# Kernel tuning notes

Measured on AMD Instinct MI355X. Metric: run time of the kernel, lower is better.

## Reference

```python
import jax, jax.numpy as jnp
import numpy as np

COLB = 16            # COL_BLOCK_WIDTH
IN_W = 1024          # input_width; zero_inputs=0 so input_locations = arange(IN_W)
OUT_W = 512          # output_width
DEPTH = 8            # network_depth
IN_L = 4             # butterfly_in_depth
OUT_L = 4            # butterfly_out_depth
ACT = 8              # activations_per_block
BLOCKS = 64          # blocks_per_layer -> num_inputs = 1024 per module
CURV = 1.0
GROW = BLOCKS * ACT  # 512 new rows per module
TOTAL = IN_W + DEPTH * GROW  # 5120
BATCH = 4096


def setup_inputs() -> dict:
    key = jax.random.key(0)
    k1, k2, k3 = jax.random.split(key, 3)
    input_data = jax.random.normal(k1, (IN_W, BATCH), dtype=jnp.float32)
    scales = jnp.full((IN_W,), 0.05, dtype=jnp.float32)
    # angles uniform in (-pi, pi), shape [depth, in_layers+out_layers, num_inputs/2]
    angles = (jax.random.uniform(k2, (DEPTH, IN_L + OUT_L, BLOCKS * COLB // 2)) * 2.0 - 1.0) * np.pi
    angles = angles.astype(jnp.float32)
    biases = jax.random.normal(k3, (DEPTH, GROW), dtype=jnp.float32) * 0.05
    # per-module indices_in = randperm(total_width_so_far)[:num_inputs]
    rng = np.random.RandomState(0)
    tw = IN_W
    idxs = []
    for _ in range(DEPTH):
        idxs.append(rng.permutation(tw)[: BLOCKS * COLB].astype(np.int32))
        tw += GROW
    indices_in = jnp.asarray(np.stack(idxs))  # [depth, 1024]
    return {"input_data": input_data, "scales": scales, "angles": angles,
            "biases": biases, "indices_in": indices_in}


def _rotate(x, ang, stride):
    # x: [W, B]; pair row i (with (i//stride)%2==0) with row i+stride inside 16-blocks
    W, B = x.shape
    xr = x.reshape(W // (2 * stride), 2, stride, B)
    a = ang.reshape(W // (2 * stride), stride)[:, :, None]
    c, s = jnp.cos(a), jnp.sin(a)
    lo, hi = xr[:, 0], xr[:, 1]              # [W/2s, s, B]
    nlo = c * lo + s * hi
    nhi = -s * lo + c * hi
    return jnp.stack([nlo, nhi], axis=1).reshape(W, B)


def _butterfly_module(data, ang, bias, idx, idx_out):
    W = BLOCKS * COLB
    x = data[idx]                             # gather [1024, B]
    for l in range(IN_L):
        x = _rotate(x, ang[l], 2 ** (l % 4))
    xb = x.reshape(BLOCKS, COLB, -1)
    pre = xb[:, :ACT, :] + bias.reshape(BLOCKS, ACT)[:, :, None]
    # curvature (smoothed-ReLU) activation
    act = 0.5 * (pre + jnp.sqrt(pre * pre + CURV * CURV))
    xb = xb.at[:, :ACT, :].set(act)
    x = xb.reshape(W, -1)
    for l in range(OUT_L):
        x = _rotate(x, ang[IN_L + l], 2 ** ((IN_L + l) % 4))
    data = data.at[idx].set(x)                # scatter working set back
    data = data.at[idx_out: idx_out + GROW].set(act.reshape(GROW, -1))
    return data


def reference(input_data, scales, angles, biases, indices_in):
    B = input_data.shape[1]
    data = jnp.zeros((TOTAL, B), dtype=input_data.dtype)
    data = data.at[:IN_W].set(scales[:, None] * input_data)
    for i in range(DEPTH):
        data = _butterfly_module(data, angles[i], biases[i], indices_in[i], IN_W + GROW * i)
    return data[TOTAL - OUT_W:]
```

## Files before the change

kernel.cpp:

```cpp
#include <hip/hip_runtime.h>
#include <math.h>

#define N_INW     1024
#define N_DEPTH   8
#define N_GROW    512
#define N_BATCH   4096
#define N_THREADS 128
#define N_LAYERS  64

typedef __attribute__((ext_vector_type(2))) float F2;
typedef decltype(__builtin_amdgcn_cvt_pkrtz(0.f, 0.f)) H2;

__global__ void precompute_cs_kernel(const float* __restrict__ angles,
                                     float* __restrict__ cs) {
    int i = blockIdx.x * blockDim.x + threadIdx.x;
    if (i < N_LAYERS * 512) {
        int g = i >> 9, p = i & 511;
        float a = angles[i];
        cs[(2 * g) * 512 + p]     = cosf(a);
        cs[(2 * g + 1) * 512 + p] = sinf(a);
    }
}

#define ADDR(r) (((r) << 3) + ((((r) >> 4)) << 2) + cpo)

#define LD2(A) ({ H2 _h = *(const H2*)(L + (A));                               \
                  F2 _v; _v.x = (float)_h.x; _v.y = (float)_h.y; _v; })
#define ST2(A, V) do { F2 _w = (V);                                            \
    *(H2*)(L + (A)) = __builtin_amdgcn_cvt_pkrtz(_w.x, _w.y); } while (0)

#define LDCS(g, CA, CB, SA, SB) do { if (USE_TABLE) {                          \
    const float4* _c = (const float4*)(cs_tab + (2*(g))*512 + (blk<<3));       \
    const float4* _s = (const float4*)(cs_tab + (2*(g)+1)*512 + (blk<<3));     \
    CA = _c[0]; CB = _c[1]; SA = _s[0]; SB = _s[1];                            \
  } else {                                                                     \
    const float4* _p = (const float4*)(angles + (g)*512 + (blk<<3));           \
    float4 _a = _p[0], _b = _p[1];                                             \
    __sincosf(_a.x, &SA.x, &CA.x); __sincosf(_a.y, &SA.y, &CA.y);              \
    __sincosf(_a.z, &SA.z, &CA.z); __sincosf(_a.w, &SA.w, &CA.w);              \
    __sincosf(_b.x, &SB.x, &CB.x); __sincosf(_b.y, &SB.y, &CB.y);              \
    __sincosf(_b.z, &SB.z, &CB.z); __sincosf(_b.w, &SB.w, &CB.w);              \
  } } while (0)

#define ROTP(LO, HI, CC, SS) do { F2 _l = LO, _h = HI;                         \
    LO = CC * _l + SS * _h; HI = CC * _h - SS * _l; } while (0)

#define ROTS1(CA,CB,SA,SB) do {                                                \
    ROTP(x0,x1,CA.x,SA.x);  ROTP(x2,x3,CA.y,SA.y);                             \
    ROTP(x4,x5,CA.z,SA.z);  ROTP(x6,x7,CA.w,SA.w);                             \
    ROTP(x8,x9,CB.x,SB.x);  ROTP(x10,x11,CB.y,SB.y);                           \
    ROTP(x12,x13,CB.z,SB.z);ROTP(x14,x15,CB.w,SB.w); } while (0)
#define ROTS2(CA,CB,SA,SB) do {                                                \
    ROTP(x0,x2,CA.x,SA.x);  ROTP(x1,x3,CA.y,SA.y);                             \
    ROTP(x4,x6,CA.z,SA.z);  ROTP(x5,x7,CA.w,SA.w);                             \
    ROTP(x8,x10,CB.x,SB.x); ROTP(x9,x11,CB.y,SB.y);                            \
    ROTP(x12,x14,CB.z,SB.z);ROTP(x13,x15,CB.w,SB.w); } while (0)
#define ROTS4(CA,CB,SA,SB) do {                                                \
    ROTP(x0,x4,CA.x,SA.x);  ROTP(x1,x5,CA.y,SA.y);                             \
    ROTP(x2,x6,CA.z,SA.z);  ROTP(x3,x7,CA.w,SA.w);                             \
    ROTP(x8,x12,CB.x,SB.x); ROTP(x9,x13,CB.y,SB.y);                            \
    ROTP(x10,x14,CB.z,SB.z);ROTP(x11,x15,CB.w,SB.w); } while (0)
#define ROTS8(CA,CB,SA,SB) do {                                                \
    ROTP(x0,x8,CA.x,SA.x);  ROTP(x1,x9,CA.y,SA.y);                             \
    ROTP(x2,x10,CA.z,SA.z); ROTP(x3,x11,CA.w,SA.w);                            \
    ROTP(x4,x12,CB.x,SB.x); ROTP(x5,x13,CB.y,SB.y);                            \
    ROTP(x6,x14,CB.z,SB.z); ROTP(x7,x15,CB.w,SB.w); } while (0)

#define ACT1(X, BB) do { F2 _p = (X) + (BB);                                   \
    F2 _t = _p * _p + 1.0f;                                                    \
    F2 _r; _r.x = __builtin_amdgcn_sqrtf(_t.x);                                \
    _r.y = __builtin_amdgcn_sqrtf(_t.y);                                       \
    X = 0.5f * (_p + _r); } while (0)

#define MODULE(M) {                                                            \
  const int a0=ADDR(i0.x), a1=ADDR(i0.y), a2=ADDR(i0.z), a3=ADDR(i0.w),        \
            a4=ADDR(i1.x), a5=ADDR(i1.y), a6=ADDR(i1.z), a7=ADDR(i1.w),        \
            a8=ADDR(i2.x), a9=ADDR(i2.y), a10=ADDR(i2.z), a11=ADDR(i2.w),      \
            a12=ADDR(i3.x), a13=ADDR(i3.y), a14=ADDR(i3.z), a15=ADDR(i3.w);    \
  float4 cA,cB,sA,sB, dA,dB,tA,tB, eA,eB,uA,uB, ba,bb;                         \
  LDCS(8*(M)+0, cA,cB,sA,sB);                                                  \
  LDCS(8*(M)+1, dA,dB,tA,tB);                                                  \
  F2 x0=LD2(a0), x1=LD2(a1), x2=LD2(a2), x3=LD2(a3);                           \
  F2 x4=LD2(a4), x5=LD2(a5), x6=LD2(a6), x7=LD2(a7);                           \
  F2 x8=LD2(a8), x9=LD2(a9), x10=LD2(a10), x11=LD2(a11);                       \
  F2 x12=LD2(a12), x13=LD2(a13), x14=LD2(a14), x15=LD2(a15);                   \
  LDCS(8*(M)+2, eA,eB,uA,uB);                                                  \
  { const float4* _bp = (const float4*)(biases + (M)*N_GROW + (blk<<3));       \
    ba = _bp[0]; bb = _bp[1]; }                                                \
  ROTS1(cA,cB,sA,sB);                                                          \
  LDCS(8*(M)+3, cA,cB,sA,sB);                                                  \
  ROTS2(dA,dB,tA,tB);                                                          \
  ROTS4(eA,eB,uA,uB);                                                          \
  ROTS8(cA,cB,sA,sB);                                                          \
  ACT1(x0,ba.x); ACT1(x1,ba.y); ACT1(x2,ba.z); ACT1(x3,ba.w);                  \
  ACT1(x4,bb.x); ACT1(x5,bb.y); ACT1(x6,bb.z); ACT1(x7,bb.w);                  \
  if ((M) < 7) {                                                               \
                            \
    const int _br = N_INW + (M)*N_GROW + (blk<<3);                             \
    const int _ab = ADDR(_br);                                                 \
    ST2(_ab+ 0,x0); ST2(_ab+ 8,x1); ST2(_ab+16,x2); ST2(_ab+24,x3);            \
    ST2(_ab+32,x4); ST2(_ab+40,x5); ST2(_ab+48,x6); ST2(_ab+56,x7);            \
                                           \
    { const int4* _ip = (const int4*)(indices + ((M)+1)*N_INW + (blk<<4));     \
      i0=_ip[0]; i1=_ip[1]; i2=_ip[2]; i3=_ip[3]; }                            \
    LDCS(8*(M)+4, dA,dB,tA,tB);                                                \
    LDCS(8*(M)+5, eA,eB,uA,uB);                                                \
    ROTS1(dA,dB,tA,tB);                                                        \
    LDCS(8*(M)+6, dA,dB,tA,tB);                                                \
    ROTS2(eA,eB,uA,uB);                                                        \
    LDCS(8*(M)+7, eA,eB,uA,uB);                                                \
    ROTS4(dA,dB,tA,tB);                                                        \
    ROTS8(eA,eB,uA,uB);                                                        \
    ST2(a0,x0);  ST2(a1,x1);  ST2(a2,x2);  ST2(a3,x3);                         \
    ST2(a4,x4);  ST2(a5,x5);  ST2(a6,x6);  ST2(a7,x7);                         \
    ST2(a8,x8);  ST2(a9,x9);  ST2(a10,x10); ST2(a11,x11);                      \
    ST2(a12,x12); ST2(a13,x13); ST2(a14,x14); ST2(a15,x15);                    \
  } else {                                                                     \
        \
    *(F2*)(out + (size_t)((blk<<3)+0)*N_BATCH + cg) = x0;                      \
    *(F2*)(out + (size_t)((blk<<3)+1)*N_BATCH + cg) = x1;                      \
    *(F2*)(out + (size_t)((blk<<3)+2)*N_BATCH + cg) = x2;                      \
    *(F2*)(out + (size_t)((blk<<3)+3)*N_BATCH + cg) = x3;                      \
    *(F2*)(out + (size_t)((blk<<3)+4)*N_BATCH + cg) = x4;                      \
    *(F2*)(out + (size_t)((blk<<3)+5)*N_BATCH + cg) = x5;                      \
    *(F2*)(out + (size_t)((blk<<3)+6)*N_BATCH + cg) = x6;                      \
    *(F2*)(out + (size_t)((blk<<3)+7)*N_BATCH + cg) = x7;                      \
  } }

template <bool USE_TABLE>
__global__ __launch_bounds__(N_THREADS, 1)
void butterfly_fused_kernel(const float* __restrict__ input,
                            const float* __restrict__ scales,
                            const float* __restrict__ biases,
                            const int*   __restrict__ indices,
                            const float* __restrict__ cs_tab,
                            const float* __restrict__ angles,
                            float* __restrict__ out) {
    extern __shared__ float ldsbuf[];
    char* L = (char*)ldsbuf;
    const int t   = threadIdx.x;
    const int blk = t & 63;
    const int cp  = t >> 6;
    const int cpo = cp << 2;
    const int b   = blockIdx.x;
    const int cg  = ((((b & 7) * 128) + (b >> 3)) << 2) + (cp << 1);

    int4 i0, i1, i2, i3;
    { const int4* ip = (const int4*)(indices + (blk << 4));
      i0 = ip[0]; i1 = ip[1]; i2 = ip[2]; i3 = ip[3]; }

#pragma unroll
    for (int k = 0; k < 16; ++k) {
        const int r = (k << 6) + blk;
        F2 v = *(const F2*)(input + (size_t)r * N_BATCH + cg);
        ST2(ADDR(r), scales[r] * v);
    }

    MODULE(0) MODULE(1) MODULE(2) MODULE(3)
    MODULE(4) MODULE(5) MODULE(6) MODULE(7)
}

extern "C" void kernel_launch(void* const* d_in, const int* in_sizes, int n_in,
                              void* d_out, int out_size, void* d_ws, size_t ws_size,
                              hipStream_t stream) {
    const float* input   = (const float*)d_in[0];
    const float* scales  = (const float*)d_in[1];
    const float* angles  = (const float*)d_in[2];
    const float* biases  = (const float*)d_in[3];
    const int*   indices = (const int*)d_in[4];
    float* out = (float*)d_out;

    const size_t cs_bytes  = (size_t)N_LAYERS * 2 * 512 * sizeof(float);
    const size_t lds_bytes = (size_t)288 * 132;
    const int grid = N_BATCH / 4;

    if (ws_size >= cs_bytes) {
        precompute_cs_kernel<<<N_LAYERS * 512 / 256, 256, 0, stream>>>(angles, (float*)d_ws);
        butterfly_fused_kernel<true><<<grid, N_THREADS, lds_bytes, stream>>>(
            input, scales, biases, indices, (const float*)d_ws, angles, out);
    } else {
        butterfly_fused_kernel<false><<<grid, N_THREADS, lds_bytes, stream>>>(
            input, scales, biases, indices, nullptr, angles, out);
    }
}
```

Before: 109.2 us.

## Software-pipeline cos/sin and bias loads one module ahead with sched barriers

Prefetches the rotation coefficient tables and biases for the next module's input layers during the current module, issues all four output-layer coefficient loads up front, and adds scheduling barriers to keep the loads ahead of the rotations. This is meant to hide global/cache load latency behind the butterfly arithmetic. The cost is many more live float4 registers, and launch bounds are changed to request two blocks per CU, which may force spilling or limit the compiler's scheduling freedom.

```diff
diff --git a/kernel.cpp b/kernel.cpp
--- a/kernel.cpp
+++ b/kernel.cpp
@@ -72,45 +72,54 @@
     _r.y = __builtin_amdgcn_sqrtf(_t.y);                                       \
     X = 0.5f * (_p + _r); } while (0)
 
+#define FENCE() __builtin_amdgcn_sched_barrier(0)
+
 #define MODULE(M) {                                                            \
   const int a0=ADDR(i0.x), a1=ADDR(i0.y), a2=ADDR(i0.z), a3=ADDR(i0.w),        \
             a4=ADDR(i1.x), a5=ADDR(i1.y), a6=ADDR(i1.z), a7=ADDR(i1.w),        \
             a8=ADDR(i2.x), a9=ADDR(i2.y), a10=ADDR(i2.z), a11=ADDR(i2.w),      \
             a12=ADDR(i3.x), a13=ADDR(i3.y), a14=ADDR(i3.z), a15=ADDR(i3.w);    \
-  float4 cA,cB,sA,sB, dA,dB,tA,tB, eA,eB,uA,uB, ba,bb;                         \
-  LDCS(8*(M)+0, cA,cB,sA,sB);                                                  \
-  LDCS(8*(M)+1, dA,dB,tA,tB);                                                  \
+              \
   F2 x0=LD2(a0), x1=LD2(a1), x2=LD2(a2), x3=LD2(a3);                           \
   F2 x4=LD2(a4), x5=LD2(a5), x6=LD2(a6), x7=LD2(a7);                           \
   F2 x8=LD2(a8), x9=LD2(a9), x10=LD2(a10), x11=LD2(a11);                       \
   F2 x12=LD2(a12), x13=LD2(a13), x14=LD2(a14), x15=LD2(a15);                   \
-  LDCS(8*(M)+2, eA,eB,uA,uB);                                                  \
-  { const float4* _bp = (const float4*)(biases + (M)*N_GROW + (blk<<3));       \
-    ba = _bp[0]; bb = _bp[1]; }                                                \
-  ROTS1(cA,cB,sA,sB);                                                          \
-  LDCS(8*(M)+3, cA,cB,sA,sB);                                                  \
-  ROTS2(dA,dB,tA,tB);                                                          \
-  ROTS4(eA,eB,uA,uB);                                                          \
-  ROTS8(cA,cB,sA,sB);                                                          \
-  ACT1(x0,ba.x); ACT1(x1,ba.y); ACT1(x2,ba.z); ACT1(x3,ba.w);                  \
-  ACT1(x4,bb.x); ACT1(x5,bb.y); ACT1(x6,bb.z); ACT1(x7,bb.w);                  \
+  float4 da0,db0,ta0,tb0, da1,db1,ta1,tb1, da2,db2,ta2,tb2, da3,db3,ta3,tb3;   \
   if ((M) < 7) {                                                               \
-                            \
+    LDCS(8*(M)+4, da0,db0,ta0,tb0);                                            \
+    LDCS(8*(M)+5, da1,db1,ta1,tb1);                                            \
+    LDCS(8*(M)+6, da2,db2,ta2,tb2);                                            \
+    LDCS(8*(M)+7, da3,db3,ta3,tb3);                                            \
+  }                                                                            \
+  FENCE();                                                                     \
+                      \
+  ROTS1(ca0,cb0,sa0,sb0);                                                      \
+  ROTS2(ca1,cb1,sa1,sb1);                                                      \
+  ROTS4(ca2,cb2,sa2,sb2);                                                      \
+  ROTS8(ca3,cb3,sa3,sb3);                                                      \
+  ACT1(x0,bA.x); ACT1(x1,bA.y); ACT1(x2,bA.z); ACT1(x3,bA.w);                  \
+  ACT1(x4,bB.x); ACT1(x5,bB.y); ACT1(x6,bB.z); ACT1(x7,bB.w);                  \
+  if ((M) < 7) {                                                               \
+                                                          \
     const int _br = N_INW + (M)*N_GROW + (blk<<3);                             \
     const int _ab = ADDR(_br);                                                 \
     ST2(_ab+ 0,x0); ST2(_ab+ 8,x1); ST2(_ab+16,x2); ST2(_ab+24,x3);            \
     ST2(_ab+32,x4); ST2(_ab+40,x5); ST2(_ab+48,x6); ST2(_ab+56,x7);            \
-                                           \
+                 \
+    LDCS(8*(M)+8,  ca0,cb0,sa0,sb0);                                           \
+    LDCS(8*(M)+9,  ca1,cb1,sa1,sb1);                                           \
+    LDCS(8*(M)+10, ca2,cb2,sa2,sb2);                                           \
+    LDCS(8*(M)+11, ca3,cb3,sa3,sb3);                                           \
     { const int4* _ip = (const int4*)(indices + ((M)+1)*N_INW + (blk<<4));     \
       i0=_ip[0]; i1=_ip[1]; i2=_ip[2]; i3=_ip[3]; }                            \
-    LDCS(8*(M)+4, dA,dB,tA,tB);                                                \
-    LDCS(8*(M)+5, eA,eB,uA,uB);                                                \
-    ROTS1(dA,dB,tA,tB);                                                        \
-    LDCS(8*(M)+6, dA,dB,tA,tB);                                                \
-    ROTS2(eA,eB,uA,uB);                                                        \
-    LDCS(8*(M)+7, eA,eB,uA,uB);                                                \
-    ROTS4(dA,dB,tA,tB);                                                        \
-    ROTS8(eA,eB,uA,uB);                                                        \
+    { const float4* _bp = (const float4*)(biases + ((M)+1)*N_GROW + (blk<<3)); \
+      bA = _bp[0]; bB = _bp[1]; }                                              \
+    FENCE();                                                                   \
+                         \
+    ROTS1(da0,db0,ta0,tb0);                                                    \
+    ROTS2(da1,db1,ta1,tb1);                                                    \
+    ROTS4(da2,db2,ta2,tb2);                                                    \
+    ROTS8(da3,db3,ta3,tb3);                                                    \
     ST2(a0,x0);  ST2(a1,x1);  ST2(a2,x2);  ST2(a3,x3);                         \
     ST2(a4,x4);  ST2(a5,x5);  ST2(a6,x6);  ST2(a7,x7);                         \
     ST2(a8,x8);  ST2(a9,x9);  ST2(a10,x10); ST2(a11,x11);                      \
@@ -128,7 +137,7 @@
   } }
 
 template <bool USE_TABLE>
-__global__ __launch_bounds__(N_THREADS, 1)
+__global__ __launch_bounds__(N_THREADS, 2)
 void butterfly_fused_kernel(const float* __restrict__ input,
                             const float* __restrict__ scales,
                             const float* __restrict__ biases,
@@ -145,9 +154,18 @@
     const int b   = blockIdx.x;
     const int cg  = ((((b & 7) * 128) + (b >> 3)) << 2) + (cp << 1);
 
+    float4 ca0,cb0,sa0,sb0, ca1,cb1,sa1,sb1, ca2,cb2,sa2,sb2, ca3,cb3,sa3,sb3;
+    float4 bA, bB;
     int4 i0, i1, i2, i3;
+
     { const int4* ip = (const int4*)(indices + (blk << 4));
       i0 = ip[0]; i1 = ip[1]; i2 = ip[2]; i3 = ip[3]; }
+    LDCS(0, ca0,cb0,sa0,sb0);
+    LDCS(1, ca1,cb1,sa1,sb1);
+    LDCS(2, ca2,cb2,sa2,sb2);
+    LDCS(3, ca3,cb3,sa3,sb3);
+    { const float4* bp = (const float4*)(biases + (blk << 3));
+      bA = bp[0]; bB = bp[1]; }
 
 #pragma unroll
     for (int k = 0; k < 16; ++k) {
```

Result: faster. 103.3 us (-5.4%).
